# Kernel optimization log

Hardware: AMD Instinct MI355X
Metric: run time of the kernel (lower is better)

The kernel has to match this reference:

```python
import jax, jax.numpy as jnp
import numpy as np

WH, WW = 8, 8
N = WH * WW            # tokens per window
DIM = 512
HEADS = 8
HD = DIM // HEADS      # head_dim = 64
SCALE = HD ** -0.5
B = 2048               # num_windows * batch


def _rel_pos_index():
    # identical to the torch buffer construction
    coords = np.stack(np.meshgrid(np.arange(WH), np.arange(WW), indexing='ij'))  # [2,WH,WW]
    flat = coords.reshape(2, -1)                          # [2,N]
    rel = (flat[:, :, None] - flat[:, None, :]).transpose(1, 2, 0)  # [N,N,2]
    rel[..., 0] += WH - 1
    rel[..., 1] += WW - 1
    rel[..., 0] *= 2 * WW - 1
    return rel.sum(-1)                                    # [N,N] int

REL_IDX = _rel_pos_index()


def setup_inputs() -> dict:
    key = jax.random.key(0)
    ks = jax.random.split(key, 16)
    f32 = jnp.float32
    return {
        'x': jax.random.normal(ks[0], (B, N, DIM), f32),
        'dino_mat': jax.random.normal(ks[1], (B, N, 384), f32),
        'point_feature': jax.random.normal(ks[2], (B, N, 3), f32),
        'color_feature': jax.random.normal(ks[3], (B, N, 3), f32),
        'shadow_detect_feature': jax.random.normal(ks[4], (B, N, 16), f32),
        'normal': jax.random.normal(ks[5], (B, N, 3), f32),
        'shadow_mask': jax.random.uniform(ks[6], (B, N, 1), dtype=f32),
        'cluster_mask': jax.random.uniform(ks[7], (B, N, 8), dtype=f32),
        'wq': jax.random.normal(ks[8], (DIM, DIM), f32) * 0.02,
        'bq': jnp.zeros((DIM,), f32),
        'wkv': jax.random.normal(ks[9], (2 * DIM, DIM), f32) * 0.02,
        'bkv': jnp.zeros((2 * DIM,), f32),
        'rel_bias_table': jax.random.normal(ks[10], ((2 * WH - 1) * (2 * WW - 1), HEADS), f32) * 0.02,
        'wproj': jax.random.normal(ks[11], (DIM, DIM), f32) * 0.02,
        'bproj': jnp.zeros((DIM,), f32),
    }


def _row_normalize(f):
    # torch: sqrt((f @ f^T per-row)).detach(), clamp(1e-20, 1e10), divide
    n = jnp.sqrt(jnp.sum(f * f, axis=-1, keepdims=True))
    n = jnp.clip(jax.lax.stop_gradient(n), 1e-20, 1e10)
    return f / n


def reference(x, dino_mat, point_feature, color_feature, shadow_detect_feature,
              normal, shadow_mask, cluster_mask, wq, bq, wkv, bkv,
              rel_bias_table, wproj, bproj):
    b = x.shape[0]
    # shadow-detect correlation map: 1 - clamp(cos-sim, 0, 1)
    sdf = _row_normalize(shadow_detect_feature)
    shadow_map = 1.0 - jnp.clip(jnp.einsum('bid,bjd->bij', sdf, sdf), 0.0, 1.0)
    # dino material correlation map
    dm = _row_normalize(dino_mat)
    dino_map = jnp.clip(jnp.einsum('bid,bjd->bij', dm, dm), 0.0, 1e10)
    # plane correlation: exp(-0.5*(|(p_i-p_j).n_i| + |(p_j-p_i).n_j|))
    diff = point_feature[:, :, None, :] - point_feature[:, None, :, :]  # [B,N,N,3]
    P = jnp.abs(jnp.sum(diff * normal[:, :, None, :], axis=-1))          # [B,N,N]
    plane_map = jnp.exp(-0.5 * (P + jnp.swapaxes(P, -1, -2)))
    # shadow mask map: 1/2 coding, outer product, ==2 -> 1 else 0.2
    sm = jnp.where(shadow_mask < 0.1, 1.0, 2.0)                          # [B,N,1]
    mm = jnp.einsum('bik,bjk->bij', sm, sm)
    mm = jnp.where(mm == 2.0, 1.0, 0.2)
    # cluster correlation map
    cc = jnp.einsum('bik,bjk->bij', cluster_mask, cluster_mask)
    # linear qkv projection (LinearProjection)
    q = (x @ wq.T + bq).reshape(b, N, HEADS, HD).transpose(0, 2, 1, 3)   # [B,H,N,d]
    kv = (x @ wkv.T + bkv).reshape(b, N, 2, HEADS, HD).transpose(2, 0, 3, 1, 4)
    k, v = kv[0], kv[1]
    attn = jnp.einsum('bhid,bhjd->bhij', q * SCALE, k)                    # [B,H,N,N]
    # all correlation maps multiply attn, broadcast over heads
    mult = shadow_map * dino_map * plane_map * cc * mm                     # [B,N,N]
    attn = attn * mult[:, None]
    # gathered relative position bias
    bias = rel_bias_table[REL_IDX.reshape(-1)].reshape(N, N, HEADS).transpose(2, 0, 1)
    attn = jax.nn.softmax(attn + bias[None], axis=-1)
    out = jnp.einsum('bhij,bhjd->bhid', attn, v)
    out = out.transpose(0, 2, 1, 3).reshape(b, N, DIM)
    return out @ wproj.T + bproj
```

## Files before the change

### kernel.cpp

```cpp
#include <hip/hip_runtime.h>

typedef unsigned short ushort_t;
typedef __bf16 bf16x8 __attribute__((ext_vector_type(8)));
typedef float f32x4 __attribute__((ext_vector_type(4)));

#define NWIN 2048
#define QKV_LD 1536
#define ATT_SCALE 0.125f

__device__ inline ushort_t f2bf(float f) {
    unsigned u = __float_as_uint(f);
    u += 0x7fffu + ((u >> 16) & 1u);
    return (ushort_t)(u >> 16);
}
__device__ inline float bl(unsigned u) { return __uint_as_float(u << 16); }
__device__ inline float bh(unsigned u) { return __uint_as_float(u & 0xffff0000u); }
__device__ inline void unpack8(uint4 u, float* f) {
    f[0] = bl(u.x); f[1] = bh(u.x); f[2] = bl(u.y); f[3] = bh(u.y);
    f[4] = bl(u.z); f[5] = bh(u.z); f[6] = bl(u.w); f[7] = bh(u.w);
}
__device__ inline float clampn(float n) { return fminf(fmaxf(n, 1e-20f), 1e10f); }

__device__ inline void async_copy16(const void* g, void* l) {
    __builtin_amdgcn_global_load_lds(
        (const __attribute__((address_space(1))) unsigned*)g,
        (__attribute__((address_space(3))) unsigned*)l, 16, 0, 0);
}

__global__ __launch_bounds__(256) void convert_x_kernel(
    const float* __restrict__ x, ushort_t* __restrict__ xbf)
{
    size_t i = ((size_t)blockIdx.x * 256 + threadIdx.x) * 8;
    float4 a = *(const float4*)&x[i];
    float4 b = *(const float4*)&x[i + 4];
    union { ushort_t us[8]; uint4 v; } p;
    p.us[0] = f2bf(a.x); p.us[1] = f2bf(a.y); p.us[2] = f2bf(a.z); p.us[3] = f2bf(a.w);
    p.us[4] = f2bf(b.x); p.us[5] = f2bf(b.y); p.us[6] = f2bf(b.z); p.us[7] = f2bf(b.w);
    *(uint4*)&xbf[i] = p.v;
}

__global__ __launch_bounds__(256) void convert_w_kernel(
    const float* __restrict__ wq, const float* __restrict__ wkv,
    ushort_t* __restrict__ wqkvbf)
{
    size_t i = ((size_t)blockIdx.x * 256 + threadIdx.x) * 8;
    const float* src = (i < 262144) ? (wq + i) : (wkv + (i - 262144));
    float4 a = *(const float4*)src;
    float4 b = *(const float4*)(src + 4);
    union { ushort_t us[8]; uint4 v; } p;
    p.us[0] = f2bf(a.x); p.us[1] = f2bf(a.y); p.us[2] = f2bf(a.z); p.us[3] = f2bf(a.w);
    p.us[4] = f2bf(b.x); p.us[5] = f2bf(b.y); p.us[6] = f2bf(b.z); p.us[7] = f2bf(b.w);
    *(uint4*)&wqkvbf[i] = p.v;
}

__global__ __launch_bounds__(256) void mult_kernel(
    const float* __restrict__ dino, const float* __restrict__ point,
    const float* __restrict__ sdf, const float* __restrict__ normal,
    const float* __restrict__ smask, const float* __restrict__ cmask,
    float* __restrict__ multo)
{
    __shared__ float chs[64][68];
    __shared__ float sdfs[64][20];
    __shared__ float pts[64][4];
    __shared__ float nrs[64][4];
    __shared__ float cls[64][12];
    __shared__ float smc[64];
    __shared__ float dinv[64];
    __shared__ float sinv[64];
    __shared__ float rpart[4][64];

    int b = blockIdx.x;
    int t = threadIdx.x;
    size_t rbase = (size_t)b * 64;

    if (t < 64) {
        int i = t;
        pts[i][0] = point[(rbase + i) * 3 + 0];
        pts[i][1] = point[(rbase + i) * 3 + 1];
        pts[i][2] = point[(rbase + i) * 3 + 2];
        nrs[i][0] = normal[(rbase + i) * 3 + 0];
        nrs[i][1] = normal[(rbase + i) * 3 + 1];
        nrs[i][2] = normal[(rbase + i) * 3 + 2];
        smc[i] = (smask[rbase + i] < 0.1f) ? 1.0f : 2.0f;
    } else if (t < 128) {
        int i = t - 64;
        float4 c0 = *(const float4*)&cmask[(rbase + i) * 8];
        float4 c1 = *(const float4*)&cmask[(rbase + i) * 8 + 4];
        cls[i][0] = c0.x; cls[i][1] = c0.y; cls[i][2] = c0.z; cls[i][3] = c0.w;
        cls[i][4] = c1.x; cls[i][5] = c1.y; cls[i][6] = c1.z; cls[i][7] = c1.w;
    } else if (t < 192) {
        int i = t - 128;
        float ss = 0.f;
        #pragma unroll
        for (int w = 0; w < 4; ++w) {
            float4 s = *(const float4*)&sdf[(rbase + i) * 16 + w * 4];
            *(float4*)&sdfs[i][w * 4] = s;
            ss += s.x * s.x + s.y * s.y + s.z * s.z + s.w * s.w;
        }
        sinv[i] = 1.0f / clampn(sqrtf(ss));
    }
    {
        int i = t & 63, part = t >> 6;
        const float* dr = dino + (rbase + i) * 384 + part * 96;
        float ss = 0.f;
        for (int d = 0; d < 96; d += 4) {
            float4 v = *(const float4*)&dr[d];
            ss += v.x * v.x + v.y * v.y + v.z * v.z + v.w * v.w;
        }
        rpart[part][i] = ss;
    }
    __syncthreads();
    if (t < 64) {
        float s = rpart[0][t] + rpart[1][t] + rpart[2][t] + rpart[3][t];
        dinv[t] = 1.0f / clampn(sqrtf(s));
    }

    int ti = t >> 4, tj = t & 15;
    int i0 = ti * 4;
    int li = t >> 2, d4 = t & 3;

    float acc[4][4] = {};
    for (int ch = 0; ch < 6; ++ch) {
        __syncthreads();
        const float* dr = dino + (rbase + li) * 384 + ch * 64 + d4 * 16;
        #pragma unroll
        for (int w = 0; w < 4; ++w)
            *(float4*)&chs[li][d4 * 16 + w * 4] = *(const float4*)&dr[w * 4];
        __syncthreads();
        #pragma unroll 4
        for (int d = 0; d < 64; d += 4) {
            float qa[4][4], kb[4][4];
            #pragma unroll
            for (int ii = 0; ii < 4; ++ii) *(float4*)qa[ii] = *(const float4*)&chs[i0 + ii][d];
            #pragma unroll
            for (int jj = 0; jj < 4; ++jj) *(float4*)kb[jj] = *(const float4*)&chs[tj + jj * 16][d];
            #pragma unroll
            for (int ii = 0; ii < 4; ++ii)
                #pragma unroll
                for (int jj = 0; jj < 4; ++jj)
                    #pragma unroll
                    for (int e = 0; e < 4; ++e)
                        acc[ii][jj] = fmaf(qa[ii][e], kb[jj][e], acc[ii][jj]);
        }
    }

    #pragma unroll
    for (int ii = 0; ii < 4; ++ii) {
        int i = i0 + ii;
        float sdI[16];
        #pragma unroll
        for (int w = 0; w < 4; ++w) *(float4*)&sdI[w * 4] = *(const float4*)&sdfs[i][w * 4];
        float pix = pts[i][0], piy = pts[i][1], piz = pts[i][2];
        float nix = nrs[i][0], niy = nrs[i][1], niz = nrs[i][2];
        float clI[8];
        *(float4*)&clI[0] = *(const float4*)&cls[i][0];
        *(float4*)&clI[4] = *(const float4*)&cls[i][4];
        float smci = smc[i], dvi = dinv[i], svi = sinv[i];
        #pragma unroll
        for (int jj = 0; jj < 4; ++jj) {
            int j = tj + jj * 16;
            float sd = 0.f;
            #pragma unroll
            for (int w = 0; w < 4; ++w) {
                float4 sj = *(const float4*)&sdfs[j][w * 4];
                sd += sdI[w * 4 + 0] * sj.x + sdI[w * 4 + 1] * sj.y +
                      sdI[w * 4 + 2] * sj.z + sdI[w * 4 + 3] * sj.w;
            }
            sd *= svi * sinv[j];
            float shadow = 1.0f - fminf(fmaxf(sd, 0.f), 1.f);
            float dd = acc[ii][jj] * dvi * dinv[j];
            float dmap = fminf(fmaxf(dd, 0.f), 1e10f);
            float dx = pix - pts[j][0], dy = piy - pts[j][1], dz = piz - pts[j][2];
            float Pij = fabsf(dx * nix + dy * niy + dz * niz);
            float Pji = fabsf(dx * nrs[j][0] + dy * nrs[j][1] + dz * nrs[j][2]);
            float plane = __expf(-0.5f * (Pij + Pji));
            float4 cj0 = *(const float4*)&cls[j][0];
            float4 cj1 = *(const float4*)&cls[j][4];
            float cc = clI[0] * cj0.x + clI[1] * cj0.y + clI[2] * cj0.z + clI[3] * cj0.w +
                       clI[4] * cj1.x + clI[5] * cj1.y + clI[6] * cj1.z + clI[7] * cj1.w;
            float mm = (smci * smc[j] == 2.0f) ? 1.0f : 0.2f;
            multo[(size_t)b * 4096 + (size_t)i * 64 + j] = shadow * dmap * plane * cc * mm;
        }
    }
}

__global__ __launch_bounds__(256) void gemm_qkv_mfma(
    const ushort_t* __restrict__ xbf, const ushort_t* __restrict__ wqkvbf,
    const float* __restrict__ bq, const float* __restrict__ bkv,
    ushort_t* __restrict__ qkv)
{
    __shared__ uint4 AsU[512];
    __shared__ uint4 BsU[512];

    int bid = blockIdx.x;
    int bx = bid % 12, by = bid / 12;
    int row0 = by * 128, col0 = bx * 128;
    const float* bias; int bcol0;
    if (bx < 4) { bias = bq;  bcol0 = col0; }
    else        { bias = bkv; bcol0 = col0 - 512; }

    int t = threadIdx.x;
    int wave = t >> 6, lane = t & 63;
    int wr = wave >> 1, wc = wave & 1;
    int l15 = lane & 15, kq = lane >> 4;

    f32x4 zero = {0.f, 0.f, 0.f, 0.f};
    f32x4 acc[4][4];
    #pragma unroll
    for (int i = 0; i < 4; ++i)
        #pragma unroll
        for (int j = 0; j < 4; ++j) acc[i][j] = zero;

    for (int k0 = 0; k0 < 512; k0 += 32) {
        #pragma unroll
        for (int q = 0; q < 2; ++q) {
            int c = wave * 128 + q * 64 + lane;
            int m = c >> 2, kg = (c & 3) ^ ((m >> 1) & 3);
            async_copy16(xbf + (size_t)(row0 + m) * 512 + k0 + kg * 8, &AsU[c]);
            async_copy16(wqkvbf + (size_t)(col0 + m) * 512 + k0 + kg * 8, &BsU[c]);
        }
        __syncthreads();
        bf16x8 af[4], bf[4];
        #pragma unroll
        for (int ii = 0; ii < 4; ++ii) {
            int M = wr * 64 + ii * 16 + l15;
            af[ii] = *(bf16x8*)&AsU[M * 4 + (kq ^ ((M >> 1) & 3))];
            int Nn = wc * 64 + ii * 16 + l15;
            bf[ii] = *(bf16x8*)&BsU[Nn * 4 + (kq ^ ((Nn >> 1) & 3))];
        }
        #pragma unroll
        for (int ii = 0; ii < 4; ++ii)
            #pragma unroll
            for (int jj = 0; jj < 4; ++jj)
                acc[ii][jj] = __builtin_amdgcn_mfma_f32_16x16x32_bf16(
                    af[ii], bf[jj], acc[ii][jj], 0, 0, 0);
        __syncthreads();
    }

    int crow = kq * 4, ccol = l15;
    #pragma unroll
    for (int ii = 0; ii < 4; ++ii) {
        #pragma unroll
        for (int jj = 0; jj < 4; ++jj) {
            int row = row0 + wr * 64 + ii * 16 + crow;
            int col = col0 + wc * 64 + jj * 16 + ccol;
            float bval = bias[col - (bcol0 >= 0 ? (col0 - bcol0) : 0) - 0];
            bval = (bias == bq) ? bq[col] : bkv[col - 512];
            #pragma unroll
            for (int r = 0; r < 4; ++r)
                qkv[(size_t)(row + r) * QKV_LD + col] = f2bf(acc[ii][jj][r] + bval);
        }
    }
}

__global__ __launch_bounds__(256) void attn_kernel(
    ushort_t* qkv, const float* __restrict__ mult, const float* __restrict__ table)
{
    __shared__ float qs[64][68];
    __shared__ float ks[64][68];
    __shared__ unsigned vsu[64][36];
    __shared__ float ps[64][68];

    int b = blockIdx.x, t = threadIdx.x;
    size_t base = (size_t)b * 64 * QKV_LD;
    int li = t >> 2, seg = t & 3;
    int ti = t >> 4, tj = t & 15;
    int i0 = ti * 4;
    int i2 = t >> 3, dq = t & 7;
    int ia = i2 * 2, ib = ia + 1, d0 = dq * 8;

    for (int h = 0; h < 8; ++h) {
        __syncthreads();
        {
            const ushort_t* row = qkv + base + (size_t)li * QKV_LD;
            uint4 u0 = *(const uint4*)(row + h * 64 + seg * 16);
            uint4 u1 = *(const uint4*)(row + h * 64 + seg * 16 + 8);
            float f[16]; unpack8(u0, f); unpack8(u1, f + 8);
            #pragma unroll
            for (int w = 0; w < 4; ++w) *(float4*)&qs[li][seg * 16 + w * 4] = *(float4*)&f[w * 4];
            uint4 k0u = *(const uint4*)(row + 512 + h * 64 + seg * 16);
            uint4 k1u = *(const uint4*)(row + 512 + h * 64 + seg * 16 + 8);
            unpack8(k0u, f); unpack8(k1u, f + 8);
            #pragma unroll
            for (int w = 0; w < 4; ++w) *(float4*)&ks[li][seg * 16 + w * 4] = *(float4*)&f[w * 4];
            uint4 v0u = *(const uint4*)(row + 1024 + h * 64 + seg * 16);
            uint4 v1u = *(const uint4*)(row + 1024 + h * 64 + seg * 16 + 8);
            *(uint4*)&vsu[li][seg * 8] = v0u;
            *(uint4*)&vsu[li][seg * 8 + 4] = v1u;
        }
        __syncthreads();

        float acc[4][4] = {};
        #pragma unroll 4
        for (int d = 0; d < 64; d += 4) {
            float qa[4][4], kb[4][4];
            #pragma unroll
            for (int ii = 0; ii < 4; ++ii) *(float4*)qa[ii] = *(const float4*)&qs[i0 + ii][d];
            #pragma unroll
            for (int jj = 0; jj < 4; ++jj) *(float4*)kb[jj] = *(const float4*)&ks[tj + jj * 16][d];
            #pragma unroll
            for (int ii = 0; ii < 4; ++ii)
                #pragma unroll
                for (int jj = 0; jj < 4; ++jj)
                    #pragma unroll
                    for (int e = 0; e < 4; ++e)
                        acc[ii][jj] = fmaf(qa[ii][e], kb[jj][e], acc[ii][jj]);
        }

        #pragma unroll
        for (int ii = 0; ii < 4; ++ii) {
            int i = i0 + ii;
            int ri = i >> 3, ci = i & 7;
            float lg[4];
            #pragma unroll
            for (int jj = 0; jj < 4; ++jj) {
                int j = tj + jj * 16;
                int rj = j >> 3, cj = j & 7;
                int idx = (ri - rj + 7) * 15 + (ci - cj + 7);
                float bias = table[idx * 8 + h];
                float m = mult[(size_t)b * 4096 + (size_t)i * 64 + j];
                lg[jj] = acc[ii][jj] * (ATT_SCALE * m) + bias;
            }
            float mx = fmaxf(fmaxf(lg[0], lg[1]), fmaxf(lg[2], lg[3]));
            #pragma unroll
            for (int s = 1; s <= 8; s <<= 1) mx = fmaxf(mx, __shfl_xor(mx, s));
            float pr[4], sum = 0.f;
            #pragma unroll
            for (int jj = 0; jj < 4; ++jj) { pr[jj] = __expf(lg[jj] - mx); sum += pr[jj]; }
            #pragma unroll
            for (int s = 1; s <= 8; s <<= 1) sum += __shfl_xor(sum, s);
            float inv = 1.0f / sum;
            #pragma unroll
            for (int jj = 0; jj < 4; ++jj) ps[i][tj + jj * 16] = pr[jj] * inv;
        }
        __syncthreads();

        float c0[8] = {}, c1[8] = {};
        #pragma unroll 4
        for (int j = 0; j < 64; ++j) {
            float a0 = ps[ia][j], a1 = ps[ib][j];
            uint4 vv = *(const uint4*)&vsu[j][dq * 4];
            float vf[8]; unpack8(vv, vf);
            #pragma unroll
            for (int e = 0; e < 8; ++e) {
                c0[e] = fmaf(a0, vf[e], c0[e]);
                c1[e] = fmaf(a1, vf[e], c1[e]);
            }
        }
        union { ushort_t us[8]; uint4 v; } p0, p1;
        #pragma unroll
        for (int e = 0; e < 8; ++e) { p0.us[e] = f2bf(c0[e]); p1.us[e] = f2bf(c1[e]); }
        *(uint4*)(qkv + base + (size_t)ia * QKV_LD + h * 64 + d0) = p0.v;
        *(uint4*)(qkv + base + (size_t)ib * QKV_LD + h * 64 + d0) = p1.v;
    }
}

__global__ __launch_bounds__(256) void gemm_proj_mfma(
    const ushort_t* __restrict__ ctx, const float* __restrict__ wproj,
    const float* __restrict__ bproj, float* __restrict__ out)
{
    __shared__ uint4 AsU[512];
    __shared__ uint4 BsU[512];

    int bid = blockIdx.x;
    int bx = bid & 3, by = bid >> 2;
    int row0 = by * 128, col0 = bx * 128;

    int t = threadIdx.x;
    int wave = t >> 6, lane = t & 63;
    int wr = wave >> 1, wc = wave & 1;
    int l15 = lane & 15, kq = lane >> 4;

    f32x4 zero = {0.f, 0.f, 0.f, 0.f};
    f32x4 acc[4][4];
    #pragma unroll
    for (int i = 0; i < 4; ++i)
        #pragma unroll
        for (int j = 0; j < 4; ++j) acc[i][j] = zero;

    for (int k0 = 0; k0 < 512; k0 += 32) {
        #pragma unroll
        for (int q = 0; q < 2; ++q) {
            int c = wave * 128 + q * 64 + lane;
            int m = c >> 2, kg = (c & 3) ^ ((m >> 1) & 3);
            async_copy16(ctx + (size_t)(row0 + m) * QKV_LD + k0 + kg * 8, &AsU[c]);
        }
        #pragma unroll
        for (int q = 0; q < 2; ++q) {
            int c = t + 256 * q;
            int n = c >> 2, kg = (c & 3) ^ ((n >> 1) & 3);
            const float* src = wproj + (size_t)(col0 + n) * 512 + k0 + kg * 8;
            float4 s0 = *(const float4*)src;
            float4 s1 = *(const float4*)(src + 4);
            union { ushort_t us[8]; uint4 v; } p;
            p.us[0] = f2bf(s0.x); p.us[1] = f2bf(s0.y); p.us[2] = f2bf(s0.z); p.us[3] = f2bf(s0.w);
            p.us[4] = f2bf(s1.x); p.us[5] = f2bf(s1.y); p.us[6] = f2bf(s1.z); p.us[7] = f2bf(s1.w);
            BsU[c] = p.v;
        }
        __syncthreads();
        bf16x8 af[4], bf[4];
        #pragma unroll
        for (int ii = 0; ii < 4; ++ii) {
            int M = wr * 64 + ii * 16 + l15;
            af[ii] = *(bf16x8*)&AsU[M * 4 + (kq ^ ((M >> 1) & 3))];
            int Nn = wc * 64 + ii * 16 + l15;
            bf[ii] = *(bf16x8*)&BsU[Nn * 4 + (kq ^ ((Nn >> 1) & 3))];
        }
        #pragma unroll
        for (int ii = 0; ii < 4; ++ii)
            #pragma unroll
            for (int jj = 0; jj < 4; ++jj)
                acc[ii][jj] = __builtin_amdgcn_mfma_f32_16x16x32_bf16(
                    af[ii], bf[jj], acc[ii][jj], 0, 0, 0);
        __syncthreads();
    }

    int crow = kq * 4, ccol = l15;
    #pragma unroll
    for (int ii = 0; ii < 4; ++ii) {
        #pragma unroll
        for (int jj = 0; jj < 4; ++jj) {
            int row = row0 + wr * 64 + ii * 16 + crow;
            int col = col0 + wc * 64 + jj * 16 + ccol;
            float bval = bproj[col];
            #pragma unroll
            for (int r = 0; r < 4; ++r)
                out[(size_t)(row + r) * 512 + col] = acc[ii][jj][r] + bval;
        }
    }
}

extern "C" void kernel_launch(void* const* d_in, const int* in_sizes, int n_in,
                              void* d_out, int out_size, void* d_ws, size_t ws_size,
                              hipStream_t stream)
{
    const float* x      = (const float*)d_in[0];
    const float* dino   = (const float*)d_in[1];
    const float* point  = (const float*)d_in[2];
    const float* sdf    = (const float*)d_in[4];
    const float* normal = (const float*)d_in[5];
    const float* smask  = (const float*)d_in[6];
    const float* cmask  = (const float*)d_in[7];
    const float* wq     = (const float*)d_in[8];
    const float* bq     = (const float*)d_in[9];
    const float* wkv    = (const float*)d_in[10];
    const float* bkv    = (const float*)d_in[11];
    const float* table  = (const float*)d_in[12];
    const float* wproj  = (const float*)d_in[13];
    const float* bproj  = (const float*)d_in[14];

    char* ob = (char*)d_out;
    ushort_t* xbf    = (ushort_t*)ob;
    ushort_t* wqkvbf = (ushort_t*)(ob + 134217728);
    float*    mult   = (float*)(ob + 136314880);
    ushort_t* qkv    = (ushort_t*)d_ws;
    float*    out    = (float*)d_out;

    hipLaunchKernelGGL(convert_x_kernel, dim3(32768), dim3(256), 0, stream, x, xbf);
    hipLaunchKernelGGL(convert_w_kernel, dim3(384), dim3(256), 0, stream, wq, wkv, wqkvbf);
    hipLaunchKernelGGL(mult_kernel, dim3(NWIN), dim3(256), 0, stream,
                       dino, point, sdf, normal, smask, cmask, mult);
    hipLaunchKernelGGL(gemm_qkv_mfma, dim3(1024 * 12), dim3(256), 0, stream,
                       xbf, wqkvbf, bq, bkv, qkv);
    hipLaunchKernelGGL(attn_kernel, dim3(NWIN), dim3(256), 0, stream,
                       qkv, mult, table);
    hipLaunchKernelGGL(gemm_proj_mfma, dim3(1024 * 4), dim3(256), 0, stream,
                       qkv, wproj, bproj, out);
}
```

Before: 1.567 ms.

## Rewrite window attention with bf16 MFMA and precomputed relative bias

Replaces the scalar fp32 attention kernel with one where each wave computes QK^T and PV for 16 query rows using bf16 MFMA 16x16x32 instructions. Q and K fragments now load straight from global memory into registers, V is transposed into LDS, and probabilities are stored in LDS as bf16. The scaled mult map is staged in LDS once per window rather than re-read for every head, and a small kernel expands the relative-position bias table into a dense per-head buffer so the per-element index arithmetic and gather go away. This cuts FMA work and LDS traffic, at the cost of rounding the probabilities to bf16 and spending extra scratch space for the bias buffer.

After: 1.406 ms. -10.3%, faster.

```diff
diff --git a/kernel.cpp b/kernel.cpp
--- a/kernel.cpp
+++ b/kernel.cpp
@@ -51,6 +51,15 @@
     p.us[0] = f2bf(a.x); p.us[1] = f2bf(a.y); p.us[2] = f2bf(a.z); p.us[3] = f2bf(a.w);
     p.us[4] = f2bf(b.x); p.us[5] = f2bf(b.y); p.us[6] = f2bf(b.z); p.us[7] = f2bf(b.w);
     *(uint4*)&wqkvbf[i] = p.v;
+}
+
+__global__ __launch_bounds__(256) void bias_expand_kernel(
+    const float* __restrict__ table, float* __restrict__ bias_full)
+{
+    int t = blockIdx.x * 256 + threadIdx.x;
+    int h = t >> 12, i = (t >> 6) & 63, j = t & 63;
+    int idx = ((i >> 3) - (j >> 3) + 7) * 15 + ((i & 7) - (j & 7) + 7);
+    bias_full[t] = table[idx * 8 + h];
 }
 
 __global__ __launch_bounds__(256) void mult_kernel(
@@ -195,9 +204,6 @@
     int bid = blockIdx.x;
     int bx = bid % 12, by = bid / 12;
     int row0 = by * 128, col0 = bx * 128;
-    const float* bias; int bcol0;
-    if (bx < 4) { bias = bq;  bcol0 = col0; }
-    else        { bias = bkv; bcol0 = col0 - 512; }
 
     int t = threadIdx.x;
     int wave = t >> 6, lane = t & 63;
@@ -237,6 +243,8 @@
         __syncthreads();
     }
 
+    const float* bq_ = bq;
+    const float* bkv_ = bkv;
     int crow = kq * 4, ccol = l15;
     #pragma unroll
     for (int ii = 0; ii < 4; ++ii) {
@@ -244,8 +252,7 @@
         for (int jj = 0; jj < 4; ++jj) {
             int row = row0 + wr * 64 + ii * 16 + crow;
             int col = col0 + wc * 64 + jj * 16 + ccol;
-            float bval = bias[col - (bcol0 >= 0 ? (col0 - bcol0) : 0) - 0];
-            bval = (bias == bq) ? bq[col] : bkv[col - 512];
+            float bval = (bx < 4) ? bq_[col] : bkv_[col - 512];
             #pragma unroll
             for (int r = 0; r < 4; ++r)
                 qkv[(size_t)(row + r) * QKV_LD + col] = f2bf(acc[ii][jj][r] + bval);
@@ -253,105 +260,109 @@
     }
 }
 
-__global__ __launch_bounds__(256) void attn_kernel(
-    ushort_t* qkv, const float* __restrict__ mult, const float* __restrict__ table)
-{
-    __shared__ float qs[64][68];
-    __shared__ float ks[64][68];
-    __shared__ unsigned vsu[64][36];
-    __shared__ float ps[64][68];
+__global__ __launch_bounds__(256) void attn_mfma_kernel(
+    ushort_t* qkv, const float* __restrict__ mult, const float* __restrict__ bias_full)
+{
+    __shared__ float multS[64][66];
+    __shared__ ushort_t vt[64][72];
+    __shared__ ushort_t ps[4][16][72];
 
     int b = blockIdx.x, t = threadIdx.x;
+    int wave = t >> 6, lane = t & 63;
+    int l15 = lane & 15, g = lane >> 4;
     size_t base = (size_t)b * 64 * QKV_LD;
-    int li = t >> 2, seg = t & 3;
-    int ti = t >> 4, tj = t & 15;
-    int i0 = ti * 4;
-    int i2 = t >> 3, dq = t & 7;
-    int ia = i2 * 2, ib = ia + 1, d0 = dq * 8;
+    const int iw0 = wave * 16;
+
+    {
+        const float* ms = mult + (size_t)b * 4096;
+        #pragma unroll
+        for (int q = 0; q < 16; ++q) {
+            int idx = q * 256 + t;
+            multS[idx >> 6][idx & 63] = ms[idx] * ATT_SCALE;
+        }
+    }
 
     for (int h = 0; h < 8; ++h) {
-        __syncthreads();
+        const ushort_t* vrow = qkv + base + (size_t)lane * QKV_LD + 1024 + h * 64 + wave * 16;
+        uint4 v0 = *(const uint4*)vrow;
+        uint4 v1 = *(const uint4*)(vrow + 8);
+
+        bf16x8 aq[2], kf[4][2];
         {
-            const ushort_t* row = qkv + base + (size_t)li * QKV_LD;
-            uint4 u0 = *(const uint4*)(row + h * 64 + seg * 16);
-            uint4 u1 = *(const uint4*)(row + h * 64 + seg * 16 + 8);
-            float f[16]; unpack8(u0, f); unpack8(u1, f + 8);
-            #pragma unroll
-            for (int w = 0; w < 4; ++w) *(float4*)&qs[li][seg * 16 + w * 4] = *(float4*)&f[w * 4];
-            uint4 k0u = *(const uint4*)(row + 512 + h * 64 + seg * 16);
-            uint4 k1u = *(const uint4*)(row + 512 + h * 64 + seg * 16 + 8);
-            unpack8(k0u, f); unpack8(k1u, f + 8);
-            #pragma unroll
-            for (int w = 0; w < 4; ++w) *(float4*)&ks[li][seg * 16 + w * 4] = *(float4*)&f[w * 4];
-            uint4 v0u = *(const uint4*)(row + 1024 + h * 64 + seg * 16);
-            uint4 v1u = *(const uint4*)(row + 1024 + h * 64 + seg * 16 + 8);
-            *(uint4*)&vsu[li][seg * 8] = v0u;
-            *(uint4*)&vsu[li][seg * 8 + 4] = v1u;
-        }
-        __syncthreads();
-
-        float acc[4][4] = {};
-        #pragma unroll 4
-        for (int d = 0; d < 64; d += 4) {
-            float qa[4][4], kb[4][4];
-            #pragma unroll
-            for (int ii = 0; ii < 4; ++ii) *(float4*)qa[ii] = *(const float4*)&qs[i0 + ii][d];
-            #pragma unroll
-            for (int jj = 0; jj < 4; ++jj) *(float4*)kb[jj] = *(const float4*)&ks[tj + jj * 16][d];
-            #pragma unroll
-            for (int ii = 0; ii < 4; ++ii)
-                #pragma unroll
-                for (int jj = 0; jj < 4; ++jj)
-                    #pragma unroll
-                    for (int e = 0; e < 4; ++e)
-                        acc[ii][jj] = fmaf(qa[ii][e], kb[jj][e], acc[ii][jj]);
-        }
-
-        #pragma unroll
-        for (int ii = 0; ii < 4; ++ii) {
-            int i = i0 + ii;
-            int ri = i >> 3, ci = i & 7;
+            const ushort_t* qb = qkv + base + (size_t)(iw0 + l15) * QKV_LD + h * 64 + g * 8;
+            aq[0] = *(const bf16x8*)qb;
+            aq[1] = *(const bf16x8*)(qb + 32);
+        }
+        #pragma unroll
+        for (int jj = 0; jj < 4; ++jj) {
+            const ushort_t* kb = qkv + base + (size_t)(jj * 16 + l15) * QKV_LD + 512 + h * 64 + g * 8;
+            kf[jj][0] = *(const bf16x8*)kb;
+            kf[jj][1] = *(const bf16x8*)(kb + 32);
+        }
+
+        {
+            union { uint4 v[2]; ushort_t us[16]; } vu;
+            vu.v[0] = v0; vu.v[1] = v1;
+            #pragma unroll
+            for (int e = 0; e < 16; ++e)
+                vt[wave * 16 + e][lane] = vu.us[e];
+        }
+        __syncthreads();
+
+        f32x4 acc[4];
+        #pragma unroll
+        for (int jj = 0; jj < 4; ++jj) acc[jj] = (f32x4){0.f, 0.f, 0.f, 0.f};
+        #pragma unroll
+        for (int kk = 0; kk < 2; ++kk)
+            #pragma unroll
+            for (int jj = 0; jj < 4; ++jj)
+                acc[jj] = __builtin_amdgcn_mfma_f32_16x16x32_bf16(
+                    aq[kk], kf[jj][kk], acc[jj], 0, 0, 0);
+
+        float invr[4];
+        #pragma unroll
+        for (int r = 0; r < 4; ++r) {
+            int iw = iw0 + g * 4 + r;
+            const float* brow = bias_full + h * 4096 + iw * 64;
             float lg[4];
             #pragma unroll
-            for (int jj = 0; jj < 4; ++jj) {
-                int j = tj + jj * 16;
-                int rj = j >> 3, cj = j & 7;
-                int idx = (ri - rj + 7) * 15 + (ci - cj + 7);
-                float bias = table[idx * 8 + h];
-                float m = mult[(size_t)b * 4096 + (size_t)i * 64 + j];
-                lg[jj] = acc[ii][jj] * (ATT_SCALE * m) + bias;
+            for (int jj = 0; jj < 4; ++jj)
+                lg[jj] = fmaf(acc[jj][r], multS[iw][jj * 16 + l15], brow[jj * 16 + l15]);
+            float mx = fmaxf(fmaxf(lg[0], lg[1]), fmaxf(lg[2], lg[3]));
+            #pragma unroll
+            for (int s = 1; s <= 8; s <<= 1) mx = fmaxf(mx, __shfl_xor(mx, s));
+            float p[4], sum = 0.f;
+            #pragma unroll
+            for (int jj = 0; jj < 4; ++jj) { p[jj] = __expf(lg[jj] - mx); sum += p[jj]; }
+            #pragma unroll
+            for (int s = 1; s <= 8; s <<= 1) sum += __shfl_xor(sum, s);
+            invr[r] = 1.0f / sum;
+            #pragma unroll
+            for (int jj = 0; jj < 4; ++jj)
+                ps[wave][g * 4 + r][jj * 16 + l15] = f2bf(p[jj]);
+        }
+
+        f32x4 po[4];
+        #pragma unroll
+        for (int dt = 0; dt < 4; ++dt) po[dt] = (f32x4){0.f, 0.f, 0.f, 0.f};
+        #pragma unroll
+        for (int kk = 0; kk < 2; ++kk) {
+            bf16x8 pa = *(const bf16x8*)&ps[wave][l15][kk * 32 + g * 8];
+            #pragma unroll
+            for (int dt = 0; dt < 4; ++dt) {
+                bf16x8 vb = *(const bf16x8*)&vt[dt * 16 + l15][kk * 32 + g * 8];
+                po[dt] = __builtin_amdgcn_mfma_f32_16x16x32_bf16(pa, vb, po[dt], 0, 0, 0);
             }
-            float mx = fmaxf(fmaxf(lg[0], lg[1]), fmaxf(lg[2], lg[3]));
-            #pragma unroll
-            for (int s = 1; s <= 8; s <<= 1) mx = fmaxf(mx, __shfl_xor(mx, s));
-            float pr[4], sum = 0.f;
-            #pragma unroll
-            for (int jj = 0; jj < 4; ++jj) { pr[jj] = __expf(lg[jj] - mx); sum += pr[jj]; }
-            #pragma unroll
-            for (int s = 1; s <= 8; s <<= 1) sum += __shfl_xor(sum, s);
-            float inv = 1.0f / sum;
-            #pragma unroll
-            for (int jj = 0; jj < 4; ++jj) ps[i][tj + jj * 16] = pr[jj] * inv;
-        }
-        __syncthreads();
-
-        float c0[8] = {}, c1[8] = {};
-        #pragma unroll 4
-        for (int j = 0; j < 64; ++j) {
-            float a0 = ps[ia][j], a1 = ps[ib][j];
-            uint4 vv = *(const uint4*)&vsu[j][dq * 4];
-            float vf[8]; unpack8(vv, vf);
-            #pragma unroll
-            for (int e = 0; e < 8; ++e) {
-                c0[e] = fmaf(a0, vf[e], c0[e]);
-                c1[e] = fmaf(a1, vf[e], c1[e]);
-            }
-        }
-        union { ushort_t us[8]; uint4 v; } p0, p1;
-        #pragma unroll
-        for (int e = 0; e < 8; ++e) { p0.us[e] = f2bf(c0[e]); p1.us[e] = f2bf(c1[e]); }
-        *(uint4*)(qkv + base + (size_t)ia * QKV_LD + h * 64 + d0) = p0.v;
-        *(uint4*)(qkv + base + (size_t)ib * QKV_LD + h * 64 + d0) = p1.v;
+        }
+
+        #pragma unroll
+        for (int dt = 0; dt < 4; ++dt)
+            #pragma unroll
+            for (int r = 0; r < 4; ++r)
+                qkv[base + (size_t)(iw0 + g * 4 + r) * QKV_LD + h * 64 + dt * 16 + l15] =
+                    f2bf(po[dt][r] * invr[r]);
+
+        __syncthreads();
     }
 }
 
@@ -450,20 +461,22 @@
     const float* bproj  = (const float*)d_in[14];
 
     char* ob = (char*)d_out;
-    ushort_t* xbf    = (ushort_t*)ob;
-    ushort_t* wqkvbf = (ushort_t*)(ob + 134217728);
-    float*    mult   = (float*)(ob + 136314880);
-    ushort_t* qkv    = (ushort_t*)d_ws;
-    float*    out    = (float*)d_out;
+    ushort_t* xbf     = (ushort_t*)ob;
+    ushort_t* wqkvbf  = (ushort_t*)(ob + 134217728);
+    float*    mult    = (float*)(ob + 136314880);
+    float*    biasf   = (float*)(ob + 169869312);
+    ushort_t* qkv     = (ushort_t*)d_ws;
+    float*    out     = (float*)d_out;
 
     hipLaunchKernelGGL(convert_x_kernel, dim3(32768), dim3(256), 0, stream, x, xbf);
     hipLaunchKernelGGL(convert_w_kernel, dim3(384), dim3(256), 0, stream, wq, wkv, wqkvbf);
+    hipLaunchKernelGGL(bias_expand_kernel, dim3(128), dim3(256), 0, stream, table, biasf);
     hipLaunchKernelGGL(mult_kernel, dim3(NWIN), dim3(256), 0, stream,
                        dino, point, sdf, normal, smask, cmask, mult);
     hipLaunchKernelGGL(gemm_qkv_mfma, dim3(1024 * 12), dim3(256), 0, stream,
                        xbf, wqkvbf, bq, bkv, qkv);
-    hipLaunchKernelGGL(attn_kernel, dim3(NWIN), dim3(256), 0, stream,
-                       qkv, mult, table);
+    hipLaunchKernelGGL(attn_mfma_kernel, dim3(NWIN), dim3(256), 0, stream,
+                       qkv, mult, biasf);
     hipLaunchKernelGGL(gemm_proj_mfma, dim3(1024 * 4), dim3(256), 0, stream,
                        qkv, wproj, bproj, out);
 }
```
